# Performance work log

Hardware: AMD Instinct MI355X
Metric: run time of the kernel (lower is better)

The kernel has to match this reference:

```python
import jax, jax.numpy as jnp
import numpy as np

TEMPERATURE = 0.1   # g.temperature
THRESHOLD = 0.05    # g.init_threshold
B, LEN_S, LEN_E = 8, 50, 10   # batch, sentence positions, max_word_length
N = B * LEN_S * LEN_E         # number of candidate spans
VOCAB = 30000


def setup_inputs() -> dict:
    key = jax.random.key(0)
    k0, k1 = jax.random.split(key)
    # positive edit-distance-like scores between every candidate span and every vocab word
    ed_dist = jax.random.uniform(k0, (N, VOCAB), dtype=jnp.float32) * 10.0
    flat = jnp.arange(N, dtype=jnp.int64)
    bi = flat // (LEN_S * LEN_E)          # batch index of each candidate
    lsi = (flat // LEN_E) % LEN_S         # start index
    lei = flat % LEN_E                    # (length-1) index
    viable = jax.random.uniform(k1, (N,)) < 0.5
    return {"ed_dist": ed_dist, "bi": bi, "lsi": lsi, "lei": lei, "viable": viable}


def _soft_min(x, axis):
    # w = (-x / T).log_softmax().exp(); value = (x * w).sum; index = argmin
    w = jax.nn.softmax(-x / TEMPERATURE, axis=axis)
    return (x * w).sum(axis), jnp.argmin(x, axis=axis)


def _soft_max(x, axis):
    w = jax.nn.softmax(x / TEMPERATURE, axis=axis)
    return (x * w).sum(axis), jnp.argmax(x, axis=axis)


def _celu(x):  # alpha = 1
    return jnp.where(x > 0, x, jnp.expm1(jnp.minimum(x, 0.0)))


def _soft_threshold(x, thresh):
    return (_celu(1.0 - 2.0 * x / thresh) + 1.0) / 2.0


def _restore_shape(tensor, bi, lsi, lei, viable, value):
    # scatter viable candidates into dense (B, LEN_S, LEN_E); non-viable go to a dump slot
    flat_idx = bi * (LEN_S * LEN_E) + lsi * LEN_E + lei
    dump = B * LEN_S * LEN_E
    idx = jnp.where(viable, flat_idx, dump)
    ret = jnp.full((dump + 1,), value, dtype=tensor.dtype)
    ret = ret.at[idx].set(tensor)
    return ret[:-1].reshape(B, LEN_S, LEN_E)


def reference(ed_dist, bi, lsi, lei, viable):
    # soft-min over vocab: best matched edit distance + hard vocab index
    matched_ed, matched_vocab = _soft_min(ed_dist, axis=-1)
    # soft thresholding to matching score
    matched_thresh = _soft_threshold(matched_ed, THRESHOLD)
    # restore dense (batch, len_s, len_e) shape
    score_dense = _restore_shape(matched_thresh, bi, lsi, lei, viable, 0.0)
    vocab_dense = _restore_shape(matched_vocab, bi, lsi, lei, viable, jnp.array(-1, matched_vocab.dtype))
    # soft-max over all spans per batch element
    flat_scores = score_dense.reshape(B, LEN_S * LEN_E)
    best_matched_score, best_idx = _soft_max(flat_scores, axis=-1)
    best_matched_vocab = jnp.take_along_axis(
        vocab_dense.reshape(B, LEN_S * LEN_E), best_idx[:, None], axis=1)[:, 0]
    start = best_idx // LEN_E
    end = start + best_idx % LEN_E
    return best_matched_score, start, end, best_matched_vocab, score_dense
```

## Files before the change

### kernel.cpp

```cpp
#include <hip/hip_runtime.h>
#include <stdint.h>

#define NROWS 4000
#define NCOLS 30000
#define NQ4   1875
#define BATCH 8
#define SPANS 500
#define LEN_E_ 10
#define KLOG2E 14.4269504088896340736f

__device__ __forceinline__ float fexp2(float x) {
    return __builtin_amdgcn_exp2f(x);
}

__device__ __forceinline__ int detect_elem_bytes(const uint8_t* __restrict__ p,
                                                 int tid) {
    __shared__ int s_count;
    if (tid == 0) s_count = 0;
    __syncthreads();
    int c = 0;
#pragma unroll
    for (int k = 0; k < 8; ++k) c += (p[tid * 8 + k] != 0);
#pragma unroll
    for (int off = 32; off > 0; off >>= 1) c += __shfl_down(c, off);
    if ((tid & 63) == 0) atomicAdd(&s_count, c);
    __syncthreads();
    int cnt = s_count;
    return cnt >= 800 ? 1 : (cnt >= 192 ? 4 : 8);
}

__device__ __forceinline__ bool viable_at(const void* __restrict__ p, int esz,
                                          int i) {
    if (esz == 1) return ((const uint8_t*)p)[i] != 0;
    if (esz == 4) return ((const uint32_t*)p)[i] != 0u;
    return ((const unsigned long long*)p)[i] != 0ull;
}

__global__ __launch_bounds__(256) void softmin_rows(
    const float* __restrict__ ed, const void* __restrict__ viable,
    float* __restrict__ out, int* __restrict__ amin) {
    const int row = blockIdx.x;
    const int tid = threadIdx.x;

    const int esz = detect_elem_bytes((const uint8_t*)viable, tid);

    const float4* __restrict__ rp =
        (const float4*)(ed + (size_t)row * NCOLS);

    float Z = 0.f, S = 0.f, mv = INFINITY;
    int   vi = 0;

    for (int j = tid; j < NQ4; j += 256) {
        float4 vv[4];
        vv[0] = rp[4 * j + 0];
        vv[1] = rp[4 * j + 1];
        vv[2] = rp[4 * j + 2];
        vv[3] = rp[4 * j + 3];
        const int base = j << 4;
#pragma unroll
        for (int q = 0; q < 4; ++q) {
#pragma unroll
            for (int c = 0; c < 4; ++c) {
                float x = (&vv[q].x)[c];
                float e = fexp2(x * -KLOG2E);
                Z += e;
                S = fmaf(x, e, S);
                bool lt = x < mv;
                mv = lt ? x : mv;
                vi = lt ? (base + q * 4 + c) : vi;
            }
        }
    }

#pragma unroll
    for (int off = 32; off > 0; off >>= 1) {
        Z += __shfl_down(Z, off);
        S += __shfl_down(S, off);
        float ov = __shfl_down(mv, off);
        int   oi = __shfl_down(vi, off);
        if (ov < mv || (ov == mv && oi < vi)) { mv = ov; vi = oi; }
    }
    __shared__ float wZ[4], wS[4], wM[4];
    __shared__ int   wI[4];
    if ((tid & 63) == 0) {
        int w = tid >> 6;
        wZ[w] = Z; wS[w] = S; wM[w] = mv; wI[w] = vi;
    }
    __syncthreads();

    if (tid == 0) {
        float Zt = 0.f, St = 0.f, m = INFINITY;
        int ii = 0;
#pragma unroll
        for (int w = 0; w < 4; ++w) {
            Zt += wZ[w]; St += wS[w];
            if (wM[w] < m || (wM[w] == m && wI[w] < ii)) { m = wM[w]; ii = wI[w]; }
        }
        float ed_v  = St / Zt;
        float z     = 1.f - 40.f * ed_v;
        float celu  = z > 0.f ? z : expm1f(z);
        float score = 0.5f * (celu + 1.f);
        amin[row]     = ii;
        out[32 + row] = viable_at(viable, esz, row) ? score : 0.f;
    }
}

__global__ __launch_bounds__(256) void span_softmax(
    const int* __restrict__ amin, float* __restrict__ out) {
    const int b   = blockIdx.x;
    const int tid = threadIdx.x;
    const float* __restrict__ sc = out + 32 + b * SPANS;

    __shared__ float sv[256];
    __shared__ int   si[256];

    float mx = -INFINITY; int ai = 0;
    for (int j = tid; j < SPANS; j += 256) {
        float x = sc[j];
        if (x > mx) { mx = x; ai = j; }
    }
    sv[tid] = mx; si[tid] = ai;
    __syncthreads();
    for (int off = 128; off > 0; off >>= 1) {
        if (tid < off) {
            float v2 = sv[tid+off]; int i2 = si[tid+off];
            if (v2 > sv[tid] || (v2 == sv[tid] && i2 < si[tid])) {
                sv[tid] = v2; si[tid] = i2;
            }
        }
        __syncthreads();
    }
    const float M    = sv[0];
    const int   best = si[0];
    __syncthreads();

    float Z = 0.f, S = 0.f;
    for (int j = tid; j < SPANS; j += 256) {
        float x = sc[j];
        float e = fexp2((x - M) * KLOG2E);
        Z += e;
        S = fmaf(x, e, S);
    }
    __shared__ float sZ[256], sS[256];
    sZ[tid] = Z; sS[tid] = S;
    __syncthreads();
    for (int off = 128; off > 0; off >>= 1) {
        if (tid < off) { sZ[tid] += sZ[tid+off]; sS[tid] += sS[tid+off]; }
        __syncthreads();
    }

    if (tid == 0) {
        int start = best / LEN_E_;
        int len   = best % LEN_E_;
        out[b]      = sS[0] / sZ[0];
        out[8 + b]  = (float)start;
        out[16 + b] = (float)(start + len);
        out[24 + b] = (M > 0.f) ? (float)amin[b * SPANS + best] : -1.f;
    }
}

extern "C" void kernel_launch(void* const* d_in, const int* in_sizes, int n_in,
                              void* d_out, int out_size, void* d_ws,
                              size_t ws_size, hipStream_t stream) {
    const float* ed     = (const float*)d_in[0];
    const void*  viable = d_in[4];
    float* out  = (float*)d_out;
    int*   amin = (int*)d_ws;

    hipLaunchKernelGGL(softmin_rows, dim3(NROWS), dim3(256), 0, stream,
                       ed, viable, out, amin);
    hipLaunchKernelGGL(span_softmax, dim3(BATCH), dim3(256), 0, stream,
                       amin, out);
}
```

Before: 91.43 us.

## Software-pipeline row loads with nontemporal loads and drop barrier-based dtype detection

Restructures the per-row softmin loop to prefetch the next 64 bytes per thread while processing the current ones, and switches the loads to nontemporal so the streamed matrix does not pollute cache. The viable-dtype detection now runs in the first wavefront only, with a shuffle reduction, which removes the shared atomic and two block barriers from every row block. The cost is higher register use from the prefetch buffers and a dependence on tid 0 sitting in the detecting wave.

```diff
diff --git a/kernel.cpp b/kernel.cpp
--- a/kernel.cpp
+++ b/kernel.cpp
@@ -9,31 +9,10 @@
 #define LEN_E_ 10
 #define KLOG2E 14.4269504088896340736f
 
+typedef float f32x4 __attribute__((ext_vector_type(4)));
+
 __device__ __forceinline__ float fexp2(float x) {
     return __builtin_amdgcn_exp2f(x);
-}
-
-__device__ __forceinline__ int detect_elem_bytes(const uint8_t* __restrict__ p,
-                                                 int tid) {
-    __shared__ int s_count;
-    if (tid == 0) s_count = 0;
-    __syncthreads();
-    int c = 0;
-#pragma unroll
-    for (int k = 0; k < 8; ++k) c += (p[tid * 8 + k] != 0);
-#pragma unroll
-    for (int off = 32; off > 0; off >>= 1) c += __shfl_down(c, off);
-    if ((tid & 63) == 0) atomicAdd(&s_count, c);
-    __syncthreads();
-    int cnt = s_count;
-    return cnt >= 800 ? 1 : (cnt >= 192 ? 4 : 8);
-}
-
-__device__ __forceinline__ bool viable_at(const void* __restrict__ p, int esz,
-                                          int i) {
-    if (esz == 1) return ((const uint8_t*)p)[i] != 0;
-    if (esz == 4) return ((const uint32_t*)p)[i] != 0u;
-    return ((const unsigned long long*)p)[i] != 0ull;
 }
 
 __global__ __launch_bounds__(256) void softmin_rows(
@@ -42,35 +21,74 @@
     const int row = blockIdx.x;
     const int tid = threadIdx.x;
 
-    const int esz = detect_elem_bytes((const uint8_t*)viable, tid);
+    int esz = 0;
+    if (tid < 64) {
+        const uint8_t* p = (const uint8_t*)viable;
+        int c = 0;
+#pragma unroll
+        for (int k = 0; k < 32; ++k) c += (p[tid * 32 + k] != 0);
+#pragma unroll
+        for (int off = 32; off > 0; off >>= 1) c += __shfl_down(c, off);
+        esz = (c >= 800) ? 1 : (c >= 192 ? 4 : 8);
+    }
 
-    const float4* __restrict__ rp =
-        (const float4*)(ed + (size_t)row * NCOLS);
+    const f32x4* __restrict__ rp =
+        (const f32x4*)(ed + (size_t)row * NCOLS);
 
     float Z = 0.f, S = 0.f, mv = INFINITY;
     int   vi = 0;
 
-    for (int j = tid; j < NQ4; j += 256) {
-        float4 vv[4];
-        vv[0] = rp[4 * j + 0];
-        vv[1] = rp[4 * j + 1];
-        vv[2] = rp[4 * j + 2];
-        vv[3] = rp[4 * j + 3];
-        const int base = j << 4;
-#pragma unroll
-        for (int q = 0; q < 4; ++q) {
-#pragma unroll
-            for (int c = 0; c < 4; ++c) {
-                float x = (&vv[q].x)[c];
-                float e = fexp2(x * -KLOG2E);
-                Z += e;
-                S = fmaf(x, e, S);
-                bool lt = x < mv;
-                mv = lt ? x : mv;
-                vi = lt ? (base + q * 4 + c) : vi;
-            }
-        }
+    int jc = tid;
+    f32x4 cur0 = __builtin_nontemporal_load(rp + 4 * jc + 0);
+    f32x4 cur1 = __builtin_nontemporal_load(rp + 4 * jc + 1);
+    f32x4 cur2 = __builtin_nontemporal_load(rp + 4 * jc + 2);
+    f32x4 cur3 = __builtin_nontemporal_load(rp + 4 * jc + 3);
+
+#define PROCESS(v0, v1, v2, v3, baseexpr)                                   \
+    do {                                                                    \
+        const int base_ = (baseexpr);                                       \
+        _Pragma("unroll")                                                   \
+        for (int c = 0; c < 4; ++c) {                                       \
+            float x = (v0)[c];                                              \
+            float e = fexp2(x * -KLOG2E);                                   \
+            Z += e; S = fmaf(x, e, S);                                      \
+            bool lt = x < mv; mv = lt ? x : mv; vi = lt ? base_ + c : vi;   \
+        }                                                                   \
+        _Pragma("unroll")                                                   \
+        for (int c = 0; c < 4; ++c) {                                       \
+            float x = (v1)[c];                                              \
+            float e = fexp2(x * -KLOG2E);                                   \
+            Z += e; S = fmaf(x, e, S);                                      \
+            bool lt = x < mv; mv = lt ? x : mv; vi = lt ? base_ + 4 + c : vi; \
+        }                                                                   \
+        _Pragma("unroll")                                                   \
+        for (int c = 0; c < 4; ++c) {                                       \
+            float x = (v2)[c];                                              \
+            float e = fexp2(x * -KLOG2E);                                   \
+            Z += e; S = fmaf(x, e, S);                                      \
+            bool lt = x < mv; mv = lt ? x : mv; vi = lt ? base_ + 8 + c : vi; \
+        }                                                                   \
+        _Pragma("unroll")                                                   \
+        for (int c = 0; c < 4; ++c) {                                       \
+            float x = (v3)[c];                                              \
+            float e = fexp2(x * -KLOG2E);                                   \
+            Z += e; S = fmaf(x, e, S);                                      \
+            bool lt = x < mv; mv = lt ? x : mv; vi = lt ? base_ + 12 + c : vi; \
+        }                                                                   \
+    } while (0)
+
+#pragma unroll 2
+    for (int jn = tid + 256; jn < NQ4; jn += 256) {
+        f32x4 nxt0 = __builtin_nontemporal_load(rp + 4 * jn + 0);
+        f32x4 nxt1 = __builtin_nontemporal_load(rp + 4 * jn + 1);
+        f32x4 nxt2 = __builtin_nontemporal_load(rp + 4 * jn + 2);
+        f32x4 nxt3 = __builtin_nontemporal_load(rp + 4 * jn + 3);
+        PROCESS(cur0, cur1, cur2, cur3, jc << 4);
+        cur0 = nxt0; cur1 = nxt1; cur2 = nxt2; cur3 = nxt3;
+        jc = jn;
     }
+    PROCESS(cur0, cur1, cur2, cur3, jc << 4);
+#undef PROCESS
 
 #pragma unroll
     for (int off = 32; off > 0; off >>= 1) {
@@ -100,8 +118,12 @@
         float z     = 1.f - 40.f * ed_v;
         float celu  = z > 0.f ? z : expm1f(z);
         float score = 0.5f * (celu + 1.f);
+        bool  viab;
+        if (esz == 1)      viab = ((const uint8_t*)viable)[row] != 0;
+        else if (esz == 4) viab = ((const uint32_t*)viable)[row] != 0u;
+        else               viab = ((const unsigned long long*)viable)[row] != 0ull;
         amin[row]     = ii;
-        out[32 + row] = viable_at(viable, esz, row) ? score : 0.f;
+        out[32 + row] = viab ? score : 0.f;
     }
 }
 
```

Result: slower. 153.2 us (+67.6%).

## Split each row's soft-min across two blocks with coalesced loads, merge in finish kernel

Applied to the files above, without the earlier changes.

Each vocab row is now handled by two blocks, one per half, giving 8000 blocks instead of 4000 to raise occupancy and load balance on a memory-bound streaming pass. The load pattern changes from per-thread contiguous 4×float4 chunks to a strided layout where each warp reads consecutive float4s, and the loop is fully unrolled with a fixed count. The viable-dtype detection moves out of the hot kernel into the finish kernel. The finish kernel merges the two partial (Z, S, min, argmin) tuples per row, computes the masked scores, and runs the span soft-max from shared memory. This adds a float4 workspace round trip per half-row.

```diff
diff --git a/kernel.cpp b/kernel.cpp
--- a/kernel.cpp
+++ b/kernel.cpp
@@ -3,7 +3,7 @@
 
 #define NROWS 4000
 #define NCOLS 30000
-#define NQ4   1875
+#define NF4H  3750
 #define BATCH 8
 #define SPANS 500
 #define LEN_E_ 10
@@ -36,41 +36,57 @@
     return ((const unsigned long long*)p)[i] != 0ull;
 }
 
-__global__ __launch_bounds__(256) void softmin_rows(
-    const float* __restrict__ ed, const void* __restrict__ viable,
-    float* __restrict__ out, int* __restrict__ amin) {
-    const int row = blockIdx.x;
+__global__ __launch_bounds__(256) void softmin_half(
+    const float* __restrict__ ed, float4* __restrict__ ws4) {
+    const int bid = blockIdx.x;
+    const int row = bid >> 1;
+    const int h   = bid & 1;
     const int tid = threadIdx.x;
 
-    const int esz = detect_elem_bytes((const uint8_t*)viable, tid);
-
     const float4* __restrict__ rp =
-        (const float4*)(ed + (size_t)row * NCOLS);
+        (const float4*)(ed + (size_t)row * NCOLS) + h * NF4H;
+    const int ebase = h * NF4H * 4;
 
     float Z = 0.f, S = 0.f, mv = INFINITY;
     int   vi = 0;
 
-    for (int j = tid; j < NQ4; j += 256) {
-        float4 vv[4];
-        vv[0] = rp[4 * j + 0];
-        vv[1] = rp[4 * j + 1];
-        vv[2] = rp[4 * j + 2];
-        vv[3] = rp[4 * j + 3];
-        const int base = j << 4;
-#pragma unroll
-        for (int q = 0; q < 4; ++q) {
-#pragma unroll
-            for (int c = 0; c < 4; ++c) {
-                float x = (&vv[q].x)[c];
-                float e = fexp2(x * -KLOG2E);
-                Z += e;
-                S = fmaf(x, e, S);
-                bool lt = x < mv;
-                mv = lt ? x : mv;
-                vi = lt ? (base + q * 4 + c) : vi;
-            }
-        }
-    }
+#define PROC4(vec, fidx)                                                    \
+    do {                                                                    \
+        const int base_ = ebase + (fidx) * 4;                               \
+        _Pragma("unroll")                                                   \
+        for (int c = 0; c < 4; ++c) {                                       \
+            float x = (&(vec).x)[c];                                        \
+            float e = fexp2(x * -KLOG2E);                                   \
+            Z += e;                                                         \
+            S = fmaf(x, e, S);                                              \
+            bool lt = x < mv;                                               \
+            mv = lt ? x : mv;                                               \
+            vi = lt ? (base_ + c) : vi;                                     \
+        }                                                                   \
+    } while (0)
+
+    for (int it = 0; it < 3; ++it) {
+        const int f0 = it * 1024 + tid;
+        float4 v0 = rp[f0 +   0];
+        float4 v1 = rp[f0 + 256];
+        float4 v2 = rp[f0 + 512];
+        float4 v3 = rp[f0 + 768];
+        PROC4(v0, f0);
+        PROC4(v1, f0 + 256);
+        PROC4(v2, f0 + 512);
+        PROC4(v3, f0 + 768);
+    }
+    {
+        float4 v0 = rp[3072 + tid];
+        float4 v1 = rp[3328 + tid];
+        PROC4(v0, 3072 + tid);
+        PROC4(v1, 3328 + tid);
+    }
+    if (tid < NF4H - 3584) {
+        float4 v0 = rp[3584 + tid];
+        PROC4(v0, 3584 + tid);
+    }
+#undef PROC4
 
 #pragma unroll
     for (int off = 32; off > 0; off >>= 1) {
@@ -96,22 +112,41 @@
             Zt += wZ[w]; St += wS[w];
             if (wM[w] < m || (wM[w] == m && wI[w] < ii)) { m = wM[w]; ii = wI[w]; }
         }
+        ws4[bid] = make_float4(Zt, St, m, __int_as_float(ii));
+    }
+}
+
+__global__ __launch_bounds__(256) void finish(
+    const void* __restrict__ viable, const float4* __restrict__ ws4,
+    float* __restrict__ out) {
+    const int b   = blockIdx.x;
+    const int tid = threadIdx.x;
+
+    const int esz = detect_elem_bytes((const uint8_t*)viable, tid);
+
+    __shared__ float sc[SPANS];
+    __shared__ int   svi[SPANS];
+
+    for (int j = tid; j < SPANS; j += 256) {
+        const int r = b * SPANS + j;
+        float4 a  = ws4[2 * r];
+        float4 c  = ws4[2 * r + 1];
+        float Zt  = a.x + c.x;
+        float St  = a.y + c.y;
+        bool useb = c.z < a.z;
+        int  vi   = __float_as_int(useb ? c.w : a.w);
         float ed_v  = St / Zt;
         float z     = 1.f - 40.f * ed_v;
         float celu  = z > 0.f ? z : expm1f(z);
         float score = 0.5f * (celu + 1.f);
-        amin[row]     = ii;
-        out[32 + row] = viable_at(viable, esz, row) ? score : 0.f;
-    }
-}
-
-__global__ __launch_bounds__(256) void span_softmax(
-    const int* __restrict__ amin, float* __restrict__ out) {
-    const int b   = blockIdx.x;
-    const int tid = threadIdx.x;
-    const float* __restrict__ sc = out + 32 + b * SPANS;
-
-    __shared__ float sv[256];
+        float msk   = viable_at(viable, esz, r) ? score : 0.f;
+        sc[j]  = msk;
+        svi[j] = vi;
+        out[32 + r] = msk;
+    }
+    __syncthreads();
+
+    __shared__ float sv[256], sZ[256], sS[256];
     __shared__ int   si[256];
 
     float mx = -INFINITY; int ai = 0;
@@ -141,7 +176,6 @@
         Z += e;
         S = fmaf(x, e, S);
     }
-    __shared__ float sZ[256], sS[256];
     sZ[tid] = Z; sS[tid] = S;
     __syncthreads();
     for (int off = 128; off > 0; off >>= 1) {
@@ -155,7 +189,7 @@
         out[b]      = sS[0] / sZ[0];
         out[8 + b]  = (float)start;
         out[16 + b] = (float)(start + len);
-        out[24 + b] = (M > 0.f) ? (float)amin[b * SPANS + best] : -1.f;
+        out[24 + b] = (M > 0.f) ? (float)svi[best] : -1.f;
     }
 }
 
@@ -164,11 +198,11 @@
                               size_t ws_size, hipStream_t stream) {
     const float* ed     = (const float*)d_in[0];
     const void*  viable = d_in[4];
-    float* out  = (float*)d_out;
-    int*   amin = (int*)d_ws;
-
-    hipLaunchKernelGGL(softmin_rows, dim3(NROWS), dim3(256), 0, stream,
-                       ed, viable, out, amin);
-    hipLaunchKernelGGL(span_softmax, dim3(BATCH), dim3(256), 0, stream,
-                       amin, out);
-}
+    float*  out = (float*)d_out;
+    float4* ws4 = (float4*)d_ws;
+
+    hipLaunchKernelGGL(softmin_half, dim3(2 * NROWS), dim3(256), 0, stream,
+                       ed, ws4);
+    hipLaunchKernelGGL(finish, dim3(BATCH), dim3(256), 0, stream,
+                       viable, ws4, out);
+}
```

Measured after the change: 93.17 us. No clear change (+1.9%).
